# Performance work log

Hardware: AMD Instinct MI355X
Metric: run time of the kernel (lower is better)

The kernel has to match this reference:

```python
import jax, jax.numpy as jnp
import numpy as np
from jax import lax

P = 8; E = 192; D_MODEL = E + 4; D_STATE = 16; D_CONV = 4; EXPAND = 2
D_INNER = EXPAND * D_MODEL  # 392
DT_RANK = -(-D_MODEL // 16)  # 13
MAX_FREQ = 32


def silu(v):
    return v * jax.nn.sigmoid(v)


def layernorm(v, g, b, eps=1e-5):
    m = v.mean(-1, keepdims=True)
    var = v.var(-1, keepdims=True)
    return (v - m) / jnp.sqrt(var + eps) * g + b


def mamba(x, in_w, conv_w, conv_b, xp_w, dt_w, dt_b, A_log, Dp, out_w):
    # Standard mamba_ssm Mamba block. x: (B, L, d_model)
    B, L, _ = x.shape
    xz = x @ in_w.T                      # (B,L,2*d_inner)
    xi, z = jnp.split(xz, 2, axis=-1)
    # depthwise causal conv1d (torch pads d_conv-1 both sides then truncates to L)
    xc = jnp.transpose(xi, (0, 2, 1))    # (B,d_inner,L)
    xc = lax.conv_general_dilated(xc, conv_w[:, None, :], (1,), [(D_CONV - 1, 0)],
                                  dimension_numbers=('NCH', 'OIH', 'NCH'),
                                  feature_group_count=D_INNER)
    xc = silu(jnp.transpose(xc, (0, 2, 1)) + conv_b)  # (B,L,d_inner)
    x_dbl = xc @ xp_w.T                  # (B,L,dt_rank+2*d_state)
    dt = x_dbl[..., :DT_RANK]
    Bm = x_dbl[..., DT_RANK:DT_RANK + D_STATE]
    Cm = x_dbl[..., DT_RANK + D_STATE:]
    delta = jax.nn.softplus(dt @ dt_w.T + dt_b)       # (B,L,d_inner)
    A = -jnp.exp(A_log)                               # (d_inner,d_state)
    deltaA = jnp.exp(delta[..., None] * A)            # (B,L,d_inner,d_state)
    deltaBu = delta[..., None] * Bm[:, :, None, :] * xc[..., None]

    def step(h, inp):
        dA, dBu, c = inp
        h = dA * h + dBu
        return h, jnp.einsum('bdn,bn->bd', h, c)

    h0 = jnp.zeros((B, D_INNER, D_STATE), x.dtype)
    _, ys = lax.scan(step, h0, (deltaA.transpose(1, 0, 2, 3),
                                deltaBu.transpose(1, 0, 2, 3),
                                Cm.transpose(1, 0, 2)))
    y = ys.transpose(1, 0, 2) + Dp * xc
    y = y * silu(z)
    return y @ out_w.T


def _mk_mamba_params(key):
    ks = jax.random.split(key, 6)
    s = 0.05
    return dict(
        in_w=jax.random.normal(ks[0], (2 * D_INNER, D_MODEL)) * s,
        conv_w=jax.random.normal(ks[1], (D_INNER, D_CONV)) * s,
        conv_b=jnp.zeros((D_INNER,)),
        xp_w=jax.random.normal(ks[2], (DT_RANK + 2 * D_STATE, D_INNER)) * s,
        dt_w=jax.random.normal(ks[3], (D_INNER, DT_RANK)) * s,
        dt_b=jax.random.normal(ks[4], (D_INNER,)) * 0.1,
        A_log=jnp.log(jnp.broadcast_to(jnp.arange(1, D_STATE + 1, dtype=jnp.float32), (D_INNER, D_STATE)) + 0.0),
        D=jnp.ones((D_INNER,)),
        out_w=jax.random.normal(ks[5], (D_MODEL, D_INNER)) * s,
    )


def setup_inputs() -> dict:
    key = jax.random.key(0)
    k = jax.random.split(key, 8)
    inp = {
        'x': jax.random.normal(k[0], (16, 3, 256, 256), dtype=jnp.float32),
        'patch_w': jax.random.normal(k[1], (E, 3, P, P)) * 0.05,
        'patch_b': jnp.zeros((E,)),
        'pe_ln_g': jnp.ones((E,)), 'pe_ln_b': jnp.zeros((E,)),
        'blk_ln_g': jnp.ones((D_MODEL,)), 'blk_ln_b': jnp.zeros((D_MODEL,)),
        'cls_w': jax.random.normal(k[2], (1, D_MODEL)) * 0.05,
        'cls_b': jnp.zeros((1,)),
    }
    for pref, kk in (('f_', k[3]), ('b_', k[4])):
        for name, val in _mk_mamba_params(kk).items():
            inp[pref + name] = val
    return inp


def reference(x, patch_w, patch_b, pe_ln_g, pe_ln_b,
              f_in_w, f_conv_w, f_conv_b, f_xp_w, f_dt_w, f_dt_b, f_A_log, f_D, f_out_w,
              b_in_w, b_conv_w, b_conv_b, b_xp_w, b_dt_w, b_dt_b, b_A_log, b_D, b_out_w,
              blk_ln_g, blk_ln_b, cls_w, cls_b):
    B, C, H, W = x.shape
    hp, wp = H // P, W // P
    # PatchEmbed: stride==kernel conv expressed as one GEMM over patches
    xp = x.reshape(B, C, hp, P, wp, P)
    tok = jnp.einsum('bchpwq,ecpq->bhwe', xp, patch_w) + patch_b
    tok = tok.reshape(B, hp * wp, E)
    tok = silu(layernorm(tok, pe_ln_g, pe_ln_b))
    # RotaryEmbedding: concat 4 positional channels
    L = hp * wp
    scale = 2 * np.pi / MAX_FREQ
    pos = jnp.arange(L, dtype=tok.dtype)[:, None] * scale
    row = (jnp.arange(L) // MAX_FREQ).astype(tok.dtype)[:, None] * scale
    cp = jnp.concatenate([jnp.sin(pos), jnp.cos(pos), jnp.sin(row), jnp.cos(row)], axis=-1)
    h = jnp.concatenate([tok, jnp.broadcast_to(cp[None], (B, L, 4))], axis=-1)  # (B,L,196)
    # BidirectionalMambaBlock
    fo = mamba(h, f_in_w, f_conv_w, f_conv_b, f_xp_w, f_dt_w, f_dt_b, f_A_log, f_D, f_out_w)
    bo = jnp.flip(mamba(jnp.flip(h, 1), b_in_w, b_conv_w, b_conv_b, b_xp_w, b_dt_w, b_dt_b, b_A_log, b_D, b_out_w), 1)
    out = (fo + bo) * 0.5
    out = silu(layernorm(out, blk_ln_g, blk_ln_b)) + h
    # Classifier: mean pool + linear (num_classes==2 -> 1 logit)
    return out.mean(1) @ cls_w.T + cls_b
```

## Files before the change

### kernel.cpp

```cpp
#include <hip/hip_runtime.h>
#include <cstdint>
#include <cstddef>

constexpr int B_   = 16;
constexpr int L_   = 1024;
constexpr int E_   = 192;
constexpr int DM   = 196;
constexpr int DI   = 392;
constexpr int DS   = 16;
constexpr int DTR  = 13;
constexpr int NTOK = B_ * L_;
constexpr int XDW  = DTR + 2 * DS;
constexpr int CH   = B_ * DI;

constexpr int KP_XZ = 224;
constexpr int KP_OP = 416;
constexpr int KP_PW = 192;

constexpr size_t HW_SZ = (size_t)NTOK * DM;
constexpr size_t DI_SZ = (size_t)NTOK * DI;

constexpr size_t O_H     = 0;
constexpr size_t O_H16   = 3211264;
constexpr size_t O_XI_F  = 5046272;
constexpr size_t O_XI_B  = 11468800;
constexpr size_t O_Z_F   = 17891328;
constexpr size_t O_Z_B   = 24313856;
constexpr size_t O_XC_F  = 30736384;
constexpr size_t O_XC_B  = 37158912;
constexpr size_t O_DTR_F = 43581440;
constexpr size_t O_DTR_B = 43794432;
constexpr size_t O_BC_F  = 44007424;
constexpr size_t O_BC_B  = 44531712;
constexpr size_t O_YS_F  = 45056000;
constexpr size_t O_YS_B  = 48267264;
constexpr size_t O_PW16  = 51478528;
constexpr size_t O_FIN16 = 51496960;
constexpr size_t O_BIN16 = 51584768;
constexpr size_t O_FOUT16= 51672576;
constexpr size_t O_BOUT16= 51713344;

typedef _Float16 half8 __attribute__((ext_vector_type(8)));
typedef _Float16 half4v __attribute__((ext_vector_type(4)));
typedef float f32x4v __attribute__((ext_vector_type(4)));

__device__ __forceinline__ float siluf(float x) {
    return x / (1.f + __expf(-x));
}
__device__ __forceinline__ float fexp2(float x) {
    return __builtin_amdgcn_exp2f(x);
}

__device__ __forceinline__ float blk_sum(float v, float* red) {
    #pragma unroll
    for (int o = 32; o > 0; o >>= 1) v += __shfl_down(v, o);
    int w = threadIdx.x >> 6;
    __syncthreads();
    if ((threadIdx.x & 63) == 0) red[w] = v;
    __syncthreads();
    return red[0] + red[1] + red[2] + red[3];
}

__global__ __launch_bounds__(256) void cvt_all(const float* __restrict__ pw,
                                               const float* __restrict__ fin,
                                               const float* __restrict__ bin,
                                               const float* __restrict__ fout,
                                               const float* __restrict__ bout,
                                               _Float16* __restrict__ dst) {
    int i = blockIdx.x * 256 + threadIdx.x;
    const float* src; int K, Kp, off;
    if (i < 36864)       { src = pw;   K = 192; Kp = 192; off = i; }
    else if (i < 212480) { src = fin;  K = 196; Kp = 224; off = i - 36864; }
    else if (i < 388096) { src = bin;  K = 196; Kp = 224; off = i - 212480; }
    else if (i < 469632) { src = fout; K = 392; Kp = 416; off = i - 388096; }
    else                 { src = bout; K = 392; Kp = 416; off = i - 469632; }
    int n = off / Kp, k = off - n * Kp;
    dst[i] = (_Float16)(k < K ? src[(size_t)n * K + k] : 0.f);
}

__global__ __launch_bounds__(256) void gather_patch(const float* __restrict__ x,
                                                    _Float16* __restrict__ Xp) {
    int i = blockIdx.x * 256 + threadIdx.x;
    int tok = i / 24, r = i - tok * 24;
    int c = r >> 3, p = r & 7;
    int b = tok >> 10, l = tok & 1023, hh = l >> 5, wv = l & 31;
    const float* src = x + (((size_t)(b * 3 + c) * 256 + hh * 8 + p) << 8) + wv * 8;
    float4 v0 = *(const float4*)src;
    float4 v1 = *(const float4*)(src + 4);
    half8 o;
    o[0] = (_Float16)v0.x; o[1] = (_Float16)v0.y; o[2] = (_Float16)v0.z; o[3] = (_Float16)v0.w;
    o[4] = (_Float16)v1.x; o[5] = (_Float16)v1.y; o[6] = (_Float16)v1.z; o[7] = (_Float16)v1.w;
    *(half8*)(Xp + (size_t)tok * 192 + c * 64 + p * 8) = o;
}

template <int MODE>
__device__ __forceinline__ void mfma_core(const _Float16* __restrict__ A,
                                          const _Float16* __restrict__ W,
                                          const float* __restrict__ bias,
                                          void* __restrict__ Cv_,
                                          int N, int Kpad, int ldc,
                                          int flip, int m_blk, int n_blk) {
    const int tid = threadIdx.x;
    const int wv = tid >> 6, lane = tid & 63;
    const int col = lane & 15, quad = lane >> 4;
    const int m_base = m_blk * 128 + wv * 32;
    const int n_base = n_blk * 64;

    int r0 = m_base + col, r1 = m_base + 16 + col;
    if (flip) {
        r0 = (r0 & ~1023) + (1023 - (r0 & 1023));
        r1 = (r1 & ~1023) + (1023 - (r1 & 1023));
    }
    const _Float16* a0p = A + (size_t)r0 * Kpad + quad * 8;
    const _Float16* a1p = A + (size_t)r1 * Kpad + quad * 8;

    const _Float16* bp[4];
    bool bok[4];
    #pragma unroll
    for (int j = 0; j < 4; ++j) {
        int n = n_base + j * 16 + col;
        bok[j] = (n < N);
        bp[j] = W + (size_t)(bok[j] ? n : 0) * Kpad + quad * 8;
    }

    f32x4v acc[2][4];
    #pragma unroll
    for (int i = 0; i < 2; ++i)
        #pragma unroll
        for (int j = 0; j < 4; ++j)
            #pragma unroll
            for (int r = 0; r < 4; ++r) acc[i][j][r] = 0.f;

    half8 bzero;
    #pragma unroll
    for (int q = 0; q < 8; ++q) bzero[q] = (_Float16)0.f;

    for (int k0 = 0; k0 < Kpad; k0 += 32) {
        half8 a0 = *(const half8*)(a0p + k0);
        half8 a1 = *(const half8*)(a1p + k0);
        #pragma unroll
        for (int j = 0; j < 4; ++j) {
            half8 bv = bzero;
            if (bok[j]) bv = *(const half8*)(bp[j] + k0);
            acc[0][j] = __builtin_amdgcn_mfma_f32_16x16x32_f16(a0, bv, acc[0][j], 0, 0, 0);
            acc[1][j] = __builtin_amdgcn_mfma_f32_16x16x32_f16(a1, bv, acc[1][j], 0, 0, 0);
        }
    }

    if constexpr (MODE == 0) {
        float* C = (float*)Cv_;
        #pragma unroll
        for (int i = 0; i < 2; ++i) {
            int mrow = m_base + i * 16 + quad * 4;
            #pragma unroll
            for (int j = 0; j < 4; ++j) {
                int n = n_base + j * 16 + col;
                if (n < N) {
                    float bv = bias ? bias[n] : 0.f;
                    #pragma unroll
                    for (int r = 0; r < 4; ++r)
                        C[(size_t)(mrow + r) * ldc + n] = acc[i][j][r] + bv;
                }
            }
        }
    } else if constexpr (MODE == 2 || MODE == 3) {
        __shared__ _Float16 cst[64 * 136];
        #pragma unroll
        for (int i = 0; i < 2; ++i) {
            int t_loc = wv * 32 + i * 16 + quad * 4;
            #pragma unroll
            for (int j = 0; j < 4; ++j) {
                int n_loc = j * 16 + col;
                half4v v;
                #pragma unroll
                for (int r = 0; r < 4; ++r) {
                    float xx = acc[i][j][r];
                    if (MODE == 3) xx = xx / (1.f + __expf(-xx));
                    v[r] = (_Float16)xx;
                }
                *(half4v*)&cst[n_loc * 136 + t_loc] = v;
            }
        }
        __syncthreads();
        const int n_loc = tid >> 2, chunk = tid & 3;
        const int n = n_base + n_loc;
        if (n < N) {
            const int bb = (m_blk * 128) >> 10;
            const int t0b = (m_blk * 128) & 1023;
            _Float16* dst = (_Float16*)Cv_ + (((size_t)(bb * N + n)) << 10) + t0b + chunk * 32;
            const _Float16* s = &cst[n_loc * 136 + chunk * 32];
            #pragma unroll
            for (int q = 0; q < 4; ++q)
                *(half8*)(dst + q * 8) = *(const half8*)(s + q * 8);
        }
    } else {
        __shared__ _Float16 cst[128 * 72];
        #pragma unroll
        for (int i = 0; i < 2; ++i) {
            #pragma unroll
            for (int j = 0; j < 4; ++j) {
                int n_loc = j * 16 + col;
                #pragma unroll
                for (int r = 0; r < 4; ++r) {
                    int m_loc = wv * 32 + i * 16 + quad * 4 + r;
                    cst[m_loc * 72 + n_loc] = (_Float16)acc[i][j][r];
                }
            }
        }
        __syncthreads();
        const int m_loc = tid >> 1, half = tid & 1;
        const int m = m_blk * 128 + m_loc;
        _Float16* C = (_Float16*)Cv_;
        const _Float16* s = &cst[m_loc * 72 + half * 32];
        if (n_base + 64 <= N) {
            _Float16* dst = C + (size_t)m * ldc + n_base + half * 32;
            #pragma unroll
            for (int q = 0; q < 4; ++q)
                *(half8*)(dst + q * 8) = *(const half8*)(s + q * 8);
        } else {
            #pragma unroll
            for (int q = 0; q < 32; ++q) {
                int n = n_base + half * 32 + q;
                if (n < N) C[(size_t)m * ldc + n] = s[q];
            }
        }
    }
}

__global__ __launch_bounds__(256) void mfma_patch(const _Float16* __restrict__ A,
                                                  const _Float16* __restrict__ W,
                                                  const float* __restrict__ bias,
                                                  float* __restrict__ C) {
    mfma_core<0>(A, W, bias, C, 192, KP_PW, 192, 0, blockIdx.x, blockIdx.y);
}

__global__ __launch_bounds__(256) void mfma_xz(const _Float16* __restrict__ A,
                                               const _Float16* __restrict__ Wf,
                                               const _Float16* __restrict__ Wb,
                                               _Float16* __restrict__ C0, _Float16* __restrict__ C1,
                                               _Float16* __restrict__ C2, _Float16* __restrict__ C3) {
    const int zi = blockIdx.z;
    const _Float16* W = (zi < 2 ? Wf : Wb) + (size_t)(zi & 1) * DI * KP_XZ;
    const int flip = zi >> 1;
    if (zi == 0)      mfma_core<2>(A, W, nullptr, C0, DI, KP_XZ, 0, flip, blockIdx.x, blockIdx.y);
    else if (zi == 1) mfma_core<3>(A, W, nullptr, C1, DI, KP_XZ, 0, flip, blockIdx.x, blockIdx.y);
    else if (zi == 2) mfma_core<2>(A, W, nullptr, C2, DI, KP_XZ, 0, flip, blockIdx.x, blockIdx.y);
    else              mfma_core<3>(A, W, nullptr, C3, DI, KP_XZ, 0, flip, blockIdx.x, blockIdx.y);
}

__global__ __launch_bounds__(256) void mfma_op(const _Float16* __restrict__ Af,
                                               const _Float16* __restrict__ Ab,
                                               const _Float16* __restrict__ Wf,
                                               const _Float16* __restrict__ Wb,
                                               _Float16* __restrict__ Cf, _Float16* __restrict__ Cb) {
    const int zi = blockIdx.z;
    mfma_core<4>(zi ? Ab : Af, zi ? Wb : Wf, nullptr, zi ? Cb : Cf,
                 DM, KP_OP, DM, 0, blockIdx.x, blockIdx.y);
}

__global__ __launch_bounds__(256) void ln_silu_pos(const float* __restrict__ tok,
                                                   const float* __restrict__ g,
                                                   const float* __restrict__ bb,
                                                   _Float16* __restrict__ h16) {
    const int w = threadIdx.x >> 6, lane = threadIdx.x & 63;
    const int t = blockIdx.x * 4 + w;
    const float* tp = tok + (size_t)t * E_;
    float v[3];
    float s1 = 0.f, s2 = 0.f;
    #pragma unroll
    for (int i = 0; i < 3; ++i) {
        v[i] = tp[lane + i * 64];
        s1 += v[i];
        s2 = fmaf(v[i], v[i], s2);
    }
    #pragma unroll
    for (int o = 32; o > 0; o >>= 1) {
        s1 += __shfl_xor(s1, o);
        s2 += __shfl_xor(s2, o);
    }
    float mean = s1 * (1.f / E_);
    float var = s2 * (1.f / E_) - mean * mean;
    float inv = rsqrtf(var + 1e-5f);
    _Float16* hq = h16 + (size_t)t * KP_XZ;
    #pragma unroll
    for (int i = 0; i < 3; ++i) {
        int e = lane + i * 64;
        float o = siluf((v[i] - mean) * inv * g[e] + bb[e]);
        hq[e] = (_Float16)o;
    }
    const int l = t & 1023;
    const float scale = 0.19634954084936207f;
    if (lane < 4) {
        float pv = (lane == 0) ? sinf(l * scale)
                 : (lane == 1) ? cosf(l * scale)
                 : (lane == 2) ? sinf((float)(l >> 5) * scale)
                 :               cosf((float)(l >> 5) * scale);
        hq[E_ + lane] = (_Float16)pv;
    } else if (lane < 32) {
        hq[192 + lane] = (_Float16)0.f;
    }
}

__global__ __launch_bounds__(256) void gemm_xdbl(const _Float16* __restrict__ xi_f,
                                                 const _Float16* __restrict__ xi_b,
                                                 const float* __restrict__ Wf,
                                                 const float* __restrict__ Wb,
                                                 const float* __restrict__ fcw,
                                                 const float* __restrict__ fcb,
                                                 const float* __restrict__ bcw,
                                                 const float* __restrict__ bcb,
                                                 float* __restrict__ dtrf,
                                                 float* __restrict__ dtrb,
                                                 float* __restrict__ bcf,
                                                 float* __restrict__ bcb2,
                                                 float* __restrict__ xcf,
                                                 float* __restrict__ xcb) {
    const int yi = blockIdx.y;
    const _Float16* xi = yi ? xi_b : xi_f;
    const float* W = yi ? Wb : Wf;
    const float* cw = yi ? bcw : fcw;
    const float* cb = yi ? bcb : fcb;
    float* dtr = yi ? dtrb : dtrf;
    float* bc = yi ? bcb2 : bcf;
    float* xc = yi ? xcb : xcf;
    __shared__ __align__(16) float As[16][68];
    __shared__ __align__(16) float Ws[16][68];
    const int m0 = blockIdx.x * 64;
    const int t = threadIdx.x;
    const int tx = t & 15, ty = t >> 4;
    float acc[4][4] = {};
    const int arow_l = t >> 2;
    const int kq = (t & 3) * 4;
    const int bb_ = m0 >> 10, tt0 = m0 & 1023;
    for (int kt = 0; kt < 25; ++kt) {
        const int k0 = kt << 4;
        {
            int kr = t >> 4, tc = t & 15;
            int kk = k0 + kr;
            float o4[4] = {0.f, 0.f, 0.f, 0.f};
            if (kk < DI) {
                const int tpos = tt0 + tc * 4;
                const _Float16* xp = xi + (((size_t)(bb_ * DI + kk)) << 10) + tpos;
                half4v cur = *(const half4v*)xp;
                half4v prv;
                if (tpos > 0) prv = *(const half4v*)(xp - 4);
                else { prv[0] = prv[1] = prv[2] = prv[3] = (_Float16)0.f; }
                float xw[7] = {(float)prv[1], (float)prv[2], (float)prv[3],
                               (float)cur[0], (float)cur[1], (float)cur[2], (float)cur[3]};
                float4 wv4 = *(const float4*)(cw + kk * 4);
                float wc[4] = {wv4.x, wv4.y, wv4.z, wv4.w};
                float bv = cb[kk];
                #pragma unroll
                for (int j = 0; j < 4; ++j) {
                    float a = bv;
                    #pragma unroll
                    for (int q = 0; q < 4; ++q) a = fmaf(xw[j + q], wc[q], a);
                    o4[j] = siluf(a);
                }
                *(float4*)(xc + (((size_t)(bb_ * DI + kk)) << 10) + tpos) =
                    *(float4*)o4;
            }
            *(float4*)&As[kr][tc * 4] = *(float4*)o4;
        }
        {
            bool okn = arow_l < XDW;
            const float* wp = W + (size_t)arow_l * DI;
            #pragma unroll
            for (int jj = 0; jj < 4; ++jj) {
                int kk = k0 + kq + jj;
                Ws[kq + jj][arow_l] = (okn && kk < DI) ? wp[kk] : 0.f;
            }
        }
        __syncthreads();
        #pragma unroll
        for (int k = 0; k < 16; ++k) {
            float av[4], wv[4];
            *(float4*)av = *(const float4*)&As[k][ty * 4];
            *(float4*)wv = *(const float4*)&Ws[k][tx * 4];
            #pragma unroll
            for (int i = 0; i < 4; ++i)
                #pragma unroll
                for (int j = 0; j < 4; ++j)
                    acc[i][j] = fmaf(av[i], wv[j], acc[i][j]);
        }
        __syncthreads();
    }
    #pragma unroll
    for (int i = 0; i < 4; ++i) {
        int m = m0 + ty * 4 + i;
        #pragma unroll
        for (int j = 0; j < 4; ++j) {
            int n = tx * 4 + j;
            float v = acc[i][j];
            if (n < DTR) dtr[(size_t)m * DTR + n] = v;
            else if (n < XDW) bc[(size_t)m * 32 + (n - DTR)] = v;
        }
    }
}

__global__ __launch_bounds__(256) void delta_kernel(
        const float* __restrict__ dtr_f, const float* __restrict__ dtr_b,
        float* __restrict__ dlT_f, float* __restrict__ dlT_b,
        const float* __restrict__ f_dt_w, const float* __restrict__ f_dt_b,
        const float* __restrict__ b_dt_w, const float* __restrict__ b_dt_b) {
    int i = blockIdx.x * 256 + threadIdx.x;
    int dir = i >= (int)DI_SZ;
    int j = dir ? i - (int)DI_SZ : i;
    int r = j >> 10, t = j & 1023;
    int b = r / DI, d = r - (r / DI) * DI;
    size_t tok = ((size_t)b << 10) + t;
    const float* xd = (dir ? dtr_b : dtr_f) + tok * DTR;
    const float* w = (dir ? b_dt_w : f_dt_w) + d * DTR;
    float acc = (dir ? b_dt_b : f_dt_b)[d];
    #pragma unroll
    for (int q = 0; q < DTR; ++q) acc = fmaf(xd[q], w[q], acc);
    float sp = fmaxf(acc, 0.f) + log1pf(__expf(-fabsf(acc)));
    (dir ? dlT_b : dlT_f)[j] = sp;
}

__global__ __launch_bounds__(256) void scan_kernel(
        const float* __restrict__ dlT_f, const float* __restrict__ dlT_b,
        const float* __restrict__ xcT_f, const float* __restrict__ xcT_b,
        const float* __restrict__ bc_f,  const float* __restrict__ bc_b,
        const _Float16* __restrict__ zT_f, const _Float16* __restrict__ zT_b,
        _Float16* __restrict__ y16_f,    _Float16* __restrict__ y16_b,
        const float* __restrict__ fA, const float* __restrict__ bA,
        const float* __restrict__ fD, const float* __restrict__ bD) {
    __shared__ float sP[8][8][16];
    __shared__ float sH[8][8][16];
    __shared__ float sI[8][8][16];
    const int tid = threadIdx.x;
    const int ni = tid & 3;
    const int c  = (tid >> 2) & 7;
    const int ch_l = tid >> 5;
    const int chain = blockIdx.x * 8 + ch_l;
    const int dir = chain >= CH;
    const int r = chain - (dir ? CH : 0);
    const int b = r / DI, d = r - (r / DI) * DI;

    const float* dlT = (dir ? dlT_b : dlT_f) + ((size_t)r << 10);
    const float* uT  = (dir ? xcT_b : xcT_f) + ((size_t)r << 10);
    const _Float16* zT = (dir ? zT_b : zT_f) + ((size_t)r << 10);
    const float* BC  = (dir ? bc_b  : bc_f)  + (((size_t)b << 10) * 32);
    _Float16* y16    = (dir ? y16_b : y16_f) + ((size_t)r << 10);
    const float* Al  = (dir ? bA : fA) + d * DS + ni * 4;
    float Av[4];
    #pragma unroll
    for (int i = 0; i < 4; ++i) Av[i] = -__expf(Al[i]) * 1.4426950408889634f;
    const float Dd = (dir ? bD : fD)[d];
    const int t0 = c << 7;

    if (c < 7) {
        float h[4] = {0.f, 0.f, 0.f, 0.f};
        float S = 0.f;
        const float* bcp = BC + t0 * 32 + ni * 4;
        const float* dp = dlT + t0;
        const float* up = uT + t0;
        for (int g = 0; g < 32; ++g) {
            float4 d4 = *(const float4*)(dp + g * 4);
            float4 u4 = *(const float4*)(up + g * 4);
            float dv[4] = {d4.x, d4.y, d4.z, d4.w};
            float uv[4] = {u4.x, u4.y, u4.z, u4.w};
            #pragma unroll
            for (int tt = 0; tt < 4; ++tt) {
                float4 B4 = *(const float4*)(bcp + tt * 32);
                float w = dv[tt] * uv[tt];
                S += dv[tt];
                float Bv[4] = {B4.x, B4.y, B4.z, B4.w};
                #pragma unroll
                for (int i = 0; i < 4; ++i)
                    h[i] = fmaf(fexp2(dv[tt] * Av[i]), h[i], w * Bv[i]);
            }
            bcp += 128;
        }
        #pragma unroll
        for (int i = 0; i < 4; ++i) {
            sP[ch_l][c][ni * 4 + i] = fexp2(S * Av[i]);
            sH[ch_l][c][ni * 4 + i] = h[i];
        }
    }
    __syncthreads();

    if (tid < 128) {
        const int ch = tid >> 4, n = tid & 15;
        float hi = 0.f;
        #pragma unroll
        for (int cc = 0; cc < 8; ++cc) {
            sI[ch][cc][n] = hi;
            if (cc < 7) hi = sH[ch][cc][n] + sP[ch][cc][n] * hi;
        }
    }
    __syncthreads();

    {
        float h[4];
        #pragma unroll
        for (int i = 0; i < 4; ++i) h[i] = sI[ch_l][c][ni * 4 + i];
        _Float16 ybuf[8] __attribute__((aligned(16)));
        half8 zb;
        const float* bcp = BC + t0 * 32 + ni * 4;
        const float* dp = dlT + t0;
        const float* up = uT + t0;
        for (int g = 0; g < 32; ++g) {
            if ((g & 7) == 0)
                zb = *(const half8*)(zT + t0 + ((g >> 3) << 5) + ni * 8);
            float4 d4 = *(const float4*)(dp + g * 4);
            float4 u4 = *(const float4*)(up + g * 4);
            float dv[4] = {d4.x, d4.y, d4.z, d4.w};
            float uv[4] = {u4.x, u4.y, u4.z, u4.w};
            float pq[4];
            #pragma unroll
            for (int tt = 0; tt < 4; ++tt) {
                float4 B4 = *(const float4*)(bcp + tt * 32);
                float4 C4 = *(const float4*)(bcp + tt * 32 + 16);
                float w = dv[tt] * uv[tt];
                float Bv[4] = {B4.x, B4.y, B4.z, B4.w};
                float Cv[4] = {C4.x, C4.y, C4.z, C4.w};
                float p = 0.f;
                #pragma unroll
                for (int i = 0; i < 4; ++i) {
                    h[i] = fmaf(fexp2(dv[tt] * Av[i]), h[i], w * Bv[i]);
                    p = fmaf(h[i], Cv[i], p);
                }
                pq[tt] = p;
            }
            bcp += 128;
            #pragma unroll
            for (int tt = 0; tt < 4; ++tt) {
                pq[tt] += __shfl_xor(pq[tt], 1);
                pq[tt] += __shfl_xor(pq[tt], 2);
            }
            if (((g >> 1) & 3) == ni) {
                const int base = (g & 1) * 4;
                #pragma unroll
                for (int tt = 0; tt < 4; ++tt)
                    ybuf[base + tt] =
                        (_Float16)((pq[tt] + Dd * uv[tt]) * (float)zb[base + tt]);
            }
            if ((g & 7) == 7)
                *(half8*)(y16 + t0 + ((g >> 3) << 5) + ni * 8) = *(half8*)ybuf;
        }
    }
}

__global__ __launch_bounds__(256) void transp_y(
        const _Float16* __restrict__ yf, const _Float16* __restrict__ yb,
        _Float16* __restrict__ of, _Float16* __restrict__ ob) {
    __shared__ _Float16 tile[64][72];
    const int dblk = blockIdx.z % 7, dir = blockIdx.z / 7;
    const int b = blockIdx.y, tb = blockIdx.x;
    const _Float16* y = dir ? yb : yf;
    _Float16* o = dir ? ob : of;
    const int d0 = dblk * 64, t0 = tb * 64;
    const int dl = threadIdx.x >> 2, ts = (threadIdx.x & 3) * 16;
    const int d = d0 + dl;
    if (d < DI) {
        const _Float16* src = y + (((size_t)(b * DI + d)) << 10) + t0 + ts;
        *(half8*)&tile[dl][ts] = *(const half8*)src;
        *(half8*)&tile[dl][ts + 8] = *(const half8*)(src + 8);
    } else {
        #pragma unroll
        for (int q = 0; q < 16; ++q) tile[dl][ts + q] = (_Float16)0.f;
    }
    __syncthreads();
    const int tl = threadIdx.x >> 2, ds = (threadIdx.x & 3) * 16;
    if (d0 + ds < KP_OP) {
        _Float16 v[16] __attribute__((aligned(16)));
        #pragma unroll
        for (int q = 0; q < 16; ++q) v[q] = tile[ds + q][tl];
        _Float16* dst = o + ((size_t)((b << 10) + t0 + tl)) * KP_OP + d0 + ds;
        *(half8*)dst = *(half8*)&v[0];
        *(half8*)(dst + 8) = *(half8*)&v[8];
    }
}

__global__ __launch_bounds__(256) void final_head(
        const _Float16* __restrict__ fo, const _Float16* __restrict__ bo,
        const _Float16* __restrict__ h16, const float* __restrict__ g,
        const float* __restrict__ bb, const float* __restrict__ cls_w,
        float* __restrict__ partial) {
    const int w = threadIdx.x >> 6, lane = threadIdx.x & 63;
    const int t = blockIdx.x * 4 + w;
    const int b = t >> 10, l = t & 1023;
    const _Float16* fp = fo + (size_t)t * DM;
    const _Float16* bp = bo + ((size_t)(b << 10) + (1023 - l)) * DM;
    const _Float16* hp = h16 + (size_t)t * KP_XZ;
    float v[4];
    float s1 = 0.f, s2 = 0.f;
    #pragma unroll
    for (int i = 0; i < 4; ++i) {
        int e = lane + i * 64;
        bool ok = (i < 3) || (lane < 4);
        float vv = ok ? 0.5f * ((float)fp[e] + (float)bp[e]) : 0.f;
        v[i] = vv;
        s1 += vv;
        s2 = fmaf(vv, vv, s2);
    }
    #pragma unroll
    for (int o = 32; o > 0; o >>= 1) {
        s1 += __shfl_xor(s1, o);
        s2 += __shfl_xor(s2, o);
    }
    float mean = s1 * (1.f / DM);
    float var = s2 * (1.f / DM) - mean * mean;
    float inv = rsqrtf(var + 1e-5f);
    float c = 0.f;
    #pragma unroll
    for (int i = 0; i < 4; ++i) {
        int e = lane + i * 64;
        bool ok = (i < 3) || (lane < 4);
        if (ok) {
            float o2 = (v[i] - mean) * inv * g[e] + bb[e];
            o2 = siluf(o2) + (float)hp[e];
            c = fmaf(o2, cls_w[e], c);
        }
    }
    #pragma unroll
    for (int o = 32; o > 0; o >>= 1) c += __shfl_xor(c, o);
    if (lane == 0) partial[t] = c;
}

__global__ __launch_bounds__(256) void head_reduce(const float* __restrict__ partial,
                                                   const float* __restrict__ cls_b,
                                                   float* __restrict__ out) {
    __shared__ float red[4];
    const int b = blockIdx.x;
    const float* p = partial + ((size_t)b << 10);
    float s = 0.f;
    for (int i = threadIdx.x; i < 1024; i += 256) s += p[i];
    s = blk_sum(s, red);
    if (threadIdx.x == 0) out[b] = s * (1.f / 1024.f) + cls_b[0];
}

extern "C" void kernel_launch(void* const* d_in, const int* in_sizes, int n_in,
                              void* d_out, int out_size, void* d_ws, size_t ws_size,
                              hipStream_t stream) {
    const float* x        = (const float*)d_in[0];
    const float* patch_w  = (const float*)d_in[1];
    const float* patch_b  = (const float*)d_in[2];
    const float* pe_g     = (const float*)d_in[3];
    const float* pe_b     = (const float*)d_in[4];
    const float* blk_g    = (const float*)d_in[5];
    const float* blk_b    = (const float*)d_in[6];
    const float* cls_w    = (const float*)d_in[7];
    const float* cls_b    = (const float*)d_in[8];
    const float* f_in_w   = (const float*)d_in[9];
    const float* f_conv_w = (const float*)d_in[10];
    const float* f_conv_b = (const float*)d_in[11];
    const float* f_xp_w   = (const float*)d_in[12];
    const float* f_dt_w   = (const float*)d_in[13];
    const float* f_dt_b   = (const float*)d_in[14];
    const float* f_A_log  = (const float*)d_in[15];
    const float* f_D      = (const float*)d_in[16];
    const float* f_out_w  = (const float*)d_in[17];
    const float* b_in_w   = (const float*)d_in[18];
    const float* b_conv_w = (const float*)d_in[19];
    const float* b_conv_b = (const float*)d_in[20];
    const float* b_xp_w   = (const float*)d_in[21];
    const float* b_dt_w   = (const float*)d_in[22];
    const float* b_dt_b   = (const float*)d_in[23];
    const float* b_A_log  = (const float*)d_in[24];
    const float* b_D      = (const float*)d_in[25];
    const float* b_out_w  = (const float*)d_in[26];

    float* ws = (float*)d_ws;
    float* out = (float*)d_out;

    _Float16* H16    = (_Float16*)(ws + O_H16);
    _Float16* XI16f  = (_Float16*)(ws + O_XI_F);
    _Float16* XI16b  = (_Float16*)(ws + O_XI_B);
    float* DLf       = ws + O_XI_F;
    float* DLb       = ws + O_XI_B;
    _Float16* FO16   = (_Float16*)(ws + O_XI_F);
    _Float16* BO16   = (_Float16*)(ws + O_XI_B);
    _Float16* ZT16f  = (_Float16*)(ws + O_Z_F);
    _Float16* ZT16b  = (_Float16*)(ws + O_Z_B);
    _Float16* YsTf16 = (_Float16*)(ws + O_Z_F);
    _Float16* YsTb16 = (_Float16*)(ws + O_Z_B);
    float* XCf       = ws + O_XC_F;
    float* XCb       = ws + O_XC_B;
    float* DTRf      = ws + O_DTR_F;
    float* DTRb      = ws + O_DTR_B;
    float* BCf       = ws + O_BC_F;
    float* BCb       = ws + O_BC_B;
    _Float16* Xp16   = (_Float16*)(ws + O_YS_F);
    float* TokRaw    = ws + O_YS_B;
    _Float16* Y16f   = (_Float16*)(ws + O_YS_F);
    _Float16* Y16b   = (_Float16*)(ws + O_YS_B);
    _Float16* PW16   = (_Float16*)(ws + O_PW16);
    _Float16* FIN16  = (_Float16*)(ws + O_FIN16);
    _Float16* BIN16  = (_Float16*)(ws + O_BIN16);
    _Float16* FOUT16 = (_Float16*)(ws + O_FOUT16);
    _Float16* BOUT16 = (_Float16*)(ws + O_BOUT16);

    cvt_all<<<2153, 256, 0, stream>>>(patch_w, f_in_w, b_in_w, f_out_w, b_out_w, PW16);

    gather_patch<<<(NTOK * 24) / 256, 256, 0, stream>>>(x, Xp16);
    mfma_patch<<<dim3(NTOK / 128, 3), 256, 0, stream>>>(Xp16, PW16, patch_b, TokRaw);
    ln_silu_pos<<<NTOK / 4, 256, 0, stream>>>(TokRaw, pe_g, pe_b, H16);

    mfma_xz<<<dim3(NTOK / 128, 7, 4), 256, 0, stream>>>(H16, FIN16, BIN16,
                                                        XI16f, ZT16f, XI16b, ZT16b);
    gemm_xdbl<<<dim3(NTOK / 64, 2), 256, 0, stream>>>(
        XI16f, XI16b, f_xp_w, b_xp_w, f_conv_w, f_conv_b, b_conv_w, b_conv_b,
        DTRf, DTRb, BCf, BCb, XCf, XCb);
    delta_kernel<<<(2 * (int)DI_SZ) / 256, 256, 0, stream>>>(
        DTRf, DTRb, DLf, DLb, f_dt_w, f_dt_b, b_dt_w, b_dt_b);
    scan_kernel<<<2 * CH / 8, 256, 0, stream>>>(
        DLf, DLb, XCf, XCb, BCf, BCb, ZT16f, ZT16b, Y16f, Y16b,
        f_A_log, b_A_log, f_D, b_D);
    transp_y<<<dim3(16, 16, 14), 256, 0, stream>>>(Y16f, Y16b, YsTf16, YsTb16);
    mfma_op<<<dim3(NTOK / 128, 4, 2), 256, 0, stream>>>(YsTf16, YsTb16,
                                                        FOUT16, BOUT16, FO16, BO16);
    final_head<<<NTOK / 4, 256, 0, stream>>>(FO16, BO16, H16, blk_g, blk_b, cls_w, XCf);
    head_reduce<<<B_, 256, 0, stream>>>(XCf, cls_b, out);
}
```

Measured before the change: 473.3 us.

## Store conv output and delta in fp16 and remap scan blocks for XCD locality

The conv+SiLU output and the softplus delta are now written as fp16 instead of fp32, which halves the bytes the delta and scan kernels write and read. The scan kernel also remaps blockIdx so that blocks sharing the same (direction, batch) B/C tile land on the same XCD (blockIdx & 7), which should improve L2 reuse of the B/C data. The cost is reduced precision on delta and u, which feed an exponentiated recurrence and could accumulate error.

```diff
diff --git a/kernel.cpp b/kernel.cpp
--- a/kernel.cpp
+++ b/kernel.cpp
@@ -313,8 +313,8 @@
                                                  float* __restrict__ dtrb,
                                                  float* __restrict__ bcf,
                                                  float* __restrict__ bcb2,
-                                                 float* __restrict__ xcf,
-                                                 float* __restrict__ xcb) {
+                                                 _Float16* __restrict__ xcf,
+                                                 _Float16* __restrict__ xcb) {
     const int yi = blockIdx.y;
     const _Float16* xi = yi ? xi_b : xi_f;
     const float* W = yi ? Wb : Wf;
@@ -322,7 +322,7 @@
     const float* cb = yi ? bcb : fcb;
     float* dtr = yi ? dtrb : dtrf;
     float* bc = yi ? bcb2 : bcf;
-    float* xc = yi ? xcb : xcf;
+    _Float16* xc = yi ? xcb : xcf;
     __shared__ __align__(16) float As[16][68];
     __shared__ __align__(16) float Ws[16][68];
     const int m0 = blockIdx.x * 64;
@@ -357,8 +357,10 @@
                     for (int q = 0; q < 4; ++q) a = fmaf(xw[j + q], wc[q], a);
                     o4[j] = siluf(a);
                 }
-                *(float4*)(xc + (((size_t)(bb_ * DI + kk)) << 10) + tpos) =
-                    *(float4*)o4;
+                half4v oc;
+                #pragma unroll
+                for (int j = 0; j < 4; ++j) oc[j] = (_Float16)o4[j];
+                *(half4v*)(xc + (((size_t)(bb_ * DI + kk)) << 10) + tpos) = oc;
             }
             *(float4*)&As[kr][tc * 4] = *(float4*)o4;
         }
@@ -400,7 +402,7 @@
 
 __global__ __launch_bounds__(256) void delta_kernel(
         const float* __restrict__ dtr_f, const float* __restrict__ dtr_b,
-        float* __restrict__ dlT_f, float* __restrict__ dlT_b,
+        _Float16* __restrict__ dlT_f, _Float16* __restrict__ dlT_b,
         const float* __restrict__ f_dt_w, const float* __restrict__ f_dt_b,
         const float* __restrict__ b_dt_w, const float* __restrict__ b_dt_b) {
     int i = blockIdx.x * 256 + threadIdx.x;
@@ -415,12 +417,12 @@
     #pragma unroll
     for (int q = 0; q < DTR; ++q) acc = fmaf(xd[q], w[q], acc);
     float sp = fmaxf(acc, 0.f) + log1pf(__expf(-fabsf(acc)));
-    (dir ? dlT_b : dlT_f)[j] = sp;
+    (dir ? dlT_b : dlT_f)[j] = (_Float16)sp;
 }
 
 __global__ __launch_bounds__(256) void scan_kernel(
-        const float* __restrict__ dlT_f, const float* __restrict__ dlT_b,
-        const float* __restrict__ xcT_f, const float* __restrict__ xcT_b,
+        const _Float16* __restrict__ dlT_f, const _Float16* __restrict__ dlT_b,
+        const _Float16* __restrict__ xcT_f, const _Float16* __restrict__ xcT_b,
         const float* __restrict__ bc_f,  const float* __restrict__ bc_b,
         const _Float16* __restrict__ zT_f, const _Float16* __restrict__ zT_b,
         _Float16* __restrict__ y16_f,    _Float16* __restrict__ y16_b,
@@ -433,13 +435,17 @@
     const int ni = tid & 3;
     const int c  = (tid >> 2) & 7;
     const int ch_l = tid >> 5;
-    const int chain = blockIdx.x * 8 + ch_l;
-    const int dir = chain >= CH;
-    const int r = chain - (dir ? CH : 0);
-    const int b = r / DI, d = r - (r / DI) * DI;
-
-    const float* dlT = (dir ? dlT_b : dlT_f) + ((size_t)r << 10);
-    const float* uT  = (dir ? xcT_b : xcT_f) + ((size_t)r << 10);
+    const int xcd = blockIdx.x & 7;
+    const int jj = blockIdx.x >> 3;
+    const int pair = xcd * 4 + jj / 49;
+    const int sub = jj % 49;
+    const int dir = pair >> 4;
+    const int b = pair & 15;
+    const int d = sub * 8 + ch_l;
+    const int r = b * DI + d;
+
+    const _Float16* dlT = (dir ? dlT_b : dlT_f) + ((size_t)r << 10);
+    const _Float16* uT  = (dir ? xcT_b : xcT_f) + ((size_t)r << 10);
     const _Float16* zT = (dir ? zT_b : zT_f) + ((size_t)r << 10);
     const float* BC  = (dir ? bc_b  : bc_f)  + (((size_t)b << 10) * 32);
     _Float16* y16    = (dir ? y16_b : y16_f) + ((size_t)r << 10);
@@ -454,13 +460,13 @@
         float h[4] = {0.f, 0.f, 0.f, 0.f};
         float S = 0.f;
         const float* bcp = BC + t0 * 32 + ni * 4;
-        const float* dp = dlT + t0;
-        const float* up = uT + t0;
+        const _Float16* dp = dlT + t0;
+        const _Float16* up = uT + t0;
         for (int g = 0; g < 32; ++g) {
-            float4 d4 = *(const float4*)(dp + g * 4);
-            float4 u4 = *(const float4*)(up + g * 4);
-            float dv[4] = {d4.x, d4.y, d4.z, d4.w};
-            float uv[4] = {u4.x, u4.y, u4.z, u4.w};
+            half4v d4h = *(const half4v*)(dp + g * 4);
+            half4v u4h = *(const half4v*)(up + g * 4);
+            float dv[4] = {(float)d4h[0], (float)d4h[1], (float)d4h[2], (float)d4h[3]};
+            float uv[4] = {(float)u4h[0], (float)u4h[1], (float)u4h[2], (float)u4h[3]};
             #pragma unroll
             for (int tt = 0; tt < 4; ++tt) {
                 float4 B4 = *(const float4*)(bcp + tt * 32);
@@ -499,15 +505,15 @@
         _Float16 ybuf[8] __attribute__((aligned(16)));
         half8 zb;
         const float* bcp = BC + t0 * 32 + ni * 4;
-        const float* dp = dlT + t0;
-        const float* up = uT + t0;
+        const _Float16* dp = dlT + t0;
+        const _Float16* up = uT + t0;
         for (int g = 0; g < 32; ++g) {
             if ((g & 7) == 0)
                 zb = *(const half8*)(zT + t0 + ((g >> 3) << 5) + ni * 8);
-            float4 d4 = *(const float4*)(dp + g * 4);
-            float4 u4 = *(const float4*)(up + g * 4);
-            float dv[4] = {d4.x, d4.y, d4.z, d4.w};
-            float uv[4] = {u4.x, u4.y, u4.z, u4.w};
+            half4v d4h = *(const half4v*)(dp + g * 4);
+            half4v u4h = *(const half4v*)(up + g * 4);
+            float dv[4] = {(float)d4h[0], (float)d4h[1], (float)d4h[2], (float)d4h[3]};
+            float uv[4] = {(float)u4h[0], (float)u4h[1], (float)u4h[2], (float)u4h[3]};
             float pq[4];
             #pragma unroll
             for (int tt = 0; tt < 4; ++tt) {
@@ -669,16 +675,17 @@
     _Float16* H16    = (_Float16*)(ws + O_H16);
     _Float16* XI16f  = (_Float16*)(ws + O_XI_F);
     _Float16* XI16b  = (_Float16*)(ws + O_XI_B);
-    float* DLf       = ws + O_XI_F;
-    float* DLb       = ws + O_XI_B;
+    _Float16* DL16f  = (_Float16*)(ws + O_XI_F);
+    _Float16* DL16b  = (_Float16*)(ws + O_XI_B);
     _Float16* FO16   = (_Float16*)(ws + O_XI_F);
     _Float16* BO16   = (_Float16*)(ws + O_XI_B);
     _Float16* ZT16f  = (_Float16*)(ws + O_Z_F);
     _Float16* ZT16b  = (_Float16*)(ws + O_Z_B);
     _Float16* YsTf16 = (_Float16*)(ws + O_Z_F);
     _Float16* YsTb16 = (_Float16*)(ws + O_Z_B);
-    float* XCf       = ws + O_XC_F;
-    float* XCb       = ws + O_XC_B;
+    _Float16* XC16f  = (_Float16*)(ws + O_XC_F);
+    _Float16* XC16b  = (_Float16*)(ws + O_XC_B);
+    float* Partial   = ws + O_XC_F;
     float* DTRf      = ws + O_DTR_F;
     float* DTRb      = ws + O_DTR_B;
     float* BCf       = ws + O_BC_F;
@@ -703,15 +710,15 @@
                                                         XI16f, ZT16f, XI16b, ZT16b);
     gemm_xdbl<<<dim3(NTOK / 64, 2), 256, 0, stream>>>(
         XI16f, XI16b, f_xp_w, b_xp_w, f_conv_w, f_conv_b, b_conv_w, b_conv_b,
-        DTRf, DTRb, BCf, BCb, XCf, XCb);
+        DTRf, DTRb, BCf, BCb, XC16f, XC16b);
     delta_kernel<<<(2 * (int)DI_SZ) / 256, 256, 0, stream>>>(
-        DTRf, DTRb, DLf, DLb, f_dt_w, f_dt_b, b_dt_w, b_dt_b);
+        DTRf, DTRb, DL16f, DL16b, f_dt_w, f_dt_b, b_dt_w, b_dt_b);
     scan_kernel<<<2 * CH / 8, 256, 0, stream>>>(
-        DLf, DLb, XCf, XCb, BCf, BCb, ZT16f, ZT16b, Y16f, Y16b,
+        DL16f, DL16b, XC16f, XC16b, BCf, BCb, ZT16f, ZT16b, Y16f, Y16b,
         f_A_log, b_A_log, f_D, b_D);
     transp_y<<<dim3(16, 16, 14), 256, 0, stream>>>(Y16f, Y16b, YsTf16, YsTb16);
     mfma_op<<<dim3(NTOK / 128, 4, 2), 256, 0, stream>>>(YsTf16, YsTb16,
                                                         FOUT16, BOUT16, FO16, BO16);
-    final_head<<<NTOK / 4, 256, 0, stream>>>(FO16, BO16, H16, blk_g, blk_b, cls_w, XCf);
-    head_reduce<<<B_, 256, 0, stream>>>(XCf, cls_b, out);
-}
+    final_head<<<NTOK / 4, 256, 0, stream>>>(FO16, BO16, H16, blk_g, blk_b, cls_w, Partial);
+    head_reduce<<<B_, 256, 0, stream>>>(Partial, cls_b, out);
+}
```

After: 474.6 us. About the same (+0.3%).
